# Performance work log

Hardware: AMD Instinct MI355X
Metric: run time of the kernel (lower is better)

Reference implementation:

```python
import jax, jax.numpy as jnp
import numpy as np

MP1, NX, P, HT, HE = 524288, 32768, 128, 128, 64


def setup_inputs() -> dict:
    key = jax.random.key(0)
    ks = jax.random.split(key, 12)
    w = lambda k, shape, fan_in: jax.random.normal(k, shape, jnp.float32) / np.sqrt(fan_in).astype(np.float32)
    a = jax.random.normal(ks[0], (MP1,), jnp.float32)
    x = jax.random.uniform(ks[1], (NX,), jnp.float32)
    t = jax.random.uniform(ks[2], (), jnp.float32)
    # DeepONet-style operator net: branch Linear(Mp1 -> p), trunk MLP (x,t) -> p
    Wb = w(ks[3], (P, MP1), MP1); bb = jnp.zeros((P,), jnp.float32)
    Wt1 = w(ks[4], (HT, 2), 2); bt1 = jnp.zeros((HT,), jnp.float32)
    Wt2 = w(ks[5], (HT, HT), HT); bt2 = jnp.zeros((HT,), jnp.float32)
    Wt3 = w(ks[6], (P, HT), HT); bt3 = jnp.zeros((P,), jnp.float32)
    # EnergyNet F(y,z): tiny smooth MLP R^2 -> R (needs 3rd-order derivatives)
    We1 = w(ks[7], (HE, 2), 2); be1 = jnp.zeros((HE,), jnp.float32)
    We2 = w(ks[8], (HE, HE), HE); be2 = jnp.zeros((HE,), jnp.float32)
    We3 = w(ks[9], (1, HE), HE); be3 = jnp.zeros((1,), jnp.float32)
    return dict(a=a, x=x, t=t, Wb=Wb, bb=bb, Wt1=Wt1, bt1=bt1, Wt2=Wt2, bt2=bt2,
                Wt3=Wt3, bt3=bt3, We1=We1, be1=be1, We2=We2, be2=be2, We3=We3, be3=be3)


def reference(a, x, t, Wb, bb, Wt1, bt1, Wt2, bt2, Wt3, bt3, We1, be1, We2, be2, We3, be3):
    # branch encoding of the input function a: (P,)
    b = Wb @ a + bb

    def u_fn(xi):  # scalar x -> scalar u(x, t)
        h = jnp.tanh(Wt1 @ jnp.stack([xi, t]) + bt1)
        h = jnp.tanh(Wt2 @ h + bt2)
        return jnp.dot(b, Wt3 @ h + bt3)

    def F(y, z):  # EnergyNet: scalar (y, z) -> scalar
        h = jnp.tanh(We1 @ jnp.stack([y, z]) + be1)
        h = jnp.tanh(We2 @ h + be2)
        return (We3 @ h + be3)[0]

    # u and its spatial derivatives, vmapped over the Nx grid points
    u = jax.vmap(u_fn)(x)
    u_x = jax.vmap(jax.grad(u_fn))(x)
    u_xx = jax.vmap(jax.grad(jax.grad(u_fn)))(x)
    u_xxx = jax.vmap(jax.grad(jax.grad(jax.grad(u_fn))))(x)

    # all needed partials of F(y, z), exactly as in the original module
    F_y = jax.grad(F)
    F_yz = jax.vmap(jax.grad(F_y, 1))(u, u_x)
    F_yy, F_yyz = jax.vmap(jax.value_and_grad(jax.grad(F_y), 1))(u, u_x)
    F_zz, (F_yzz, F_zzz) = jax.vmap(jax.value_and_grad(jax.grad(jax.grad(F, 1), 1), (0, 1)))(u, u_x)

    F_yx = F_yy * u_x + F_yz * u_xx
    F_zxx = (F_yz * u_xx + F_zz * u_xxx + F_yyz * u_x ** 2
             + 2.0 * F_yzz * u_x * u_xx + F_zzz * u_xx ** 2)
    return (-F_yx + F_zxx).reshape(x.shape[0])
```

## Files before the change

kernel.cpp:

```cpp
#include <hip/hip_runtime.h>
#include <cmath>

#define MP1 524288
#define NXP 32768

typedef float vfloat4 __attribute__((ext_vector_type(4)));


__global__ __launch_bounds__(256) void prep1_k(const float* __restrict__ Wt2,
                                               const float* __restrict__ We2,
                                               float* __restrict__ ws) {
    int idx = blockIdx.x * 256 + threadIdx.x;
    if (idx < 128) ws[idx] = 0.0f;
    if (idx < 16384) {
        int j = idx >> 7, k = idx & 127;
        ws[512 + k * 128 + j] = Wt2[idx];
    }
    if (idx < 4096) {
        int m = idx >> 6, i = idx & 63;
        ws[16896 + i * 64 + m] = We2[idx];
    }
}

__global__ __launch_bounds__(256) void gemv_k(const float* __restrict__ Wb,
                                              const float* __restrict__ a,
                                              float* __restrict__ b_acc) {
    const int row = blockIdx.x;
    const int chunk = blockIdx.y;
    const int t = threadIdx.x;
    size_t base = (size_t)row * MP1 + (size_t)chunk * 16384;
    const vfloat4* W4 = (const vfloat4*)(Wb + base);
    const float4* A4 = (const float4*)(a + (size_t)chunk * 16384);
    float sum = 0.0f;
#pragma unroll
    for (int it = 0; it < 16; ++it) {
        vfloat4 w = __builtin_nontemporal_load(&W4[t + it * 256]);
        float4 av = A4[t + it * 256];
        sum += w[0] * av.x + w[1] * av.y + w[2] * av.z + w[3] * av.w;
    }
#pragma unroll
    for (int off = 32; off > 0; off >>= 1) sum += __shfl_down(sum, off, 64);
    __shared__ float red[4];
    int wid = t >> 6;
    if ((t & 63) == 0) red[wid] = sum;
    __syncthreads();
    if (t == 0) atomicAdd(&b_acc[row], red[0] + red[1] + red[2] + red[3]);
}

__global__ __launch_bounds__(128) void prep2_k(const float* __restrict__ ws_in,
                                               const float* __restrict__ bb,
                                               const float* __restrict__ Wt3,
                                               const float* __restrict__ bt3,
                                               float* __restrict__ ws) {
    int k = threadIdx.x;
    float cv = 0.0f;
    for (int j = 0; j < 128; ++j)
        cv = fmaf(ws_in[j] + bb[j], Wt3[j * 128 + k], cv);
    ws[128 + k] = cv;
    float p = (ws_in[k] + bb[k]) * bt3[k];
#pragma unroll
    for (int off = 32; off > 0; off >>= 1) p += __shfl_down(p, off, 64);
    __shared__ float red[2];
    if ((k & 63) == 0) red[k >> 6] = p;
    __syncthreads();
    if (k == 0) ws[256] = red[0] + red[1];
}

#define SW_WT1 0
#define SW_BT1 256
#define SW_BT2 384
#define SW_CVEC 512
#define SW_WE1 640
#define SW_BE1 768
#define SW_BE2 832
#define SW_WE3 896
#define UREDP 960
#define H1V_ 1216
#define FREDP (H1V_ + 4096)
#define SCR_ 9408
#define LDSF 13504

__global__ __launch_bounds__(512, 4) void point_k(const float* __restrict__ x,
                                                  const float* __restrict__ tptr,
                                                  const float* __restrict__ Wt1,
                                                  const float* __restrict__ bt1,
                                                  const float* __restrict__ bt2,
                                                  const float* __restrict__ We1,
                                                  const float* __restrict__ be1,
                                                  const float* __restrict__ be2,
                                                  const float* __restrict__ We3,
                                                  const float* __restrict__ ws,
                                                  float* __restrict__ out) {
    __shared__ __align__(16) float lds[LDSF];
    const int tid = threadIdx.x;
    const int p = tid & 63;
    const int slice = __builtin_amdgcn_readfirstlane(tid >> 6);
    const int i = blockIdx.x * 64 + p;
    const float xi = x[i];
    const float tt = tptr[0];
    const float u_const = ws[256];

    if (tid < 256) lds[SW_WT1 + tid] = Wt1[tid];
    else if (tid < 384) lds[SW_BT1 + tid - 256] = bt1[tid - 256];
    else lds[SW_BT2 + tid - 384] = bt2[tid - 384];
    {
        int o = 512 + tid;
        if (o < 640) lds[o] = ws[128 + (o - 512)];
        else if (o < 768) lds[o] = We1[o - 640];
        else if (o < 832) lds[o] = be1[o - 768];
        else if (o < 896) lds[o] = be2[o - 832];
        else if (o < 960) lds[o] = We3[o - 896];
    }
    __syncthreads();

#pragma unroll
    for (int q = 0; q < 16; ++q) {
        int k = slice * 16 + q;
        float z = fmaf(lds[SW_WT1 + 2 * k], xi,
                       fmaf(lds[SW_WT1 + 2 * k + 1], tt, lds[SW_BT1 + k]));
        lds[H1V_ + k * 64 + p] = tanhf(z);
    }

    float a0[16], a1[16], a2[16], a3[16];
#pragma unroll
    for (int jj = 0; jj < 16; ++jj) { a0[jj] = 0.f; a1[jj] = 0.f; a2[jj] = 0.f; a3[jj] = 0.f; }
    for (int c = 0; c < 4; ++c) {
        __syncthreads();
        {
            const float4* src = (const float4*)(ws + 512 + c * 4096);
            float4* dst = (float4*)(lds + SCR_);
            dst[tid] = src[tid];
            dst[tid + 512] = src[tid + 512];
        }
        __syncthreads();
#pragma unroll 2
        for (int kl = 0; kl < 32; ++kl) {
            int k = c * 32 + kl;
            float v = lds[H1V_ + k * 64 + p];
            float w = lds[SW_WT1 + 2 * k];
            float s = 1.f - v * v;
            float f2 = -2.f * v * s;
            float f3 = 2.f * s * (2.f * v * v - s);
            float w2 = w * w;
            float d1 = s * w;
            float d2 = f2 * w2;
            float d3 = f3 * w2 * w;
            const float4* wr = (const float4*)(lds + SCR_ + kl * 128 + slice * 16);
            float4 wv0 = wr[0], wv1 = wr[1], wv2 = wr[2], wv3 = wr[3];
            const float wf[16] = {wv0.x, wv0.y, wv0.z, wv0.w, wv1.x, wv1.y, wv1.z, wv1.w,
                                  wv2.x, wv2.y, wv2.z, wv2.w, wv3.x, wv3.y, wv3.z, wv3.w};
#pragma unroll
            for (int jj = 0; jj < 16; ++jj) {
                float wjk = wf[jj];
                a0[jj] = fmaf(wjk, v, a0[jj]);
                a1[jj] = fmaf(wjk, d1, a1[jj]);
                a2[jj] = fmaf(wjk, d2, a2[jj]);
                a3[jj] = fmaf(wjk, d3, a3[jj]);
            }
        }
    }
    float u0 = 0.f, u1 = 0.f, u2 = 0.f, u3 = 0.f;
#pragma unroll
    for (int jj = 0; jj < 16; ++jj) {
        int j = slice * 16 + jj;
        float z0 = a0[jj] + lds[SW_BT2 + j];
        float z1 = a1[jj], z2 = a2[jj], z3 = a3[jj];
        float v = tanhf(z0);
        float s = 1.f - v * v;
        float f2 = -2.f * v * s;
        float f3 = 2.f * s * (2.f * v * v - s);
        float cj = lds[SW_CVEC + j];
        u0 = fmaf(cj, v, u0);
        u1 = fmaf(cj, s * z1, u1);
        u2 = fmaf(cj, f2 * z1 * z1 + s * z2, u2);
        u3 = fmaf(cj, f3 * z1 * z1 * z1 + 3.f * f2 * z1 * z2 + s * z3, u3);
    }
    __syncthreads();
    lds[SCR_ + 0 * 512 + slice * 64 + p] = u0;
    lds[SCR_ + 1 * 512 + slice * 64 + p] = u1;
    lds[SCR_ + 2 * 512 + slice * 64 + p] = u2;
    lds[SCR_ + 3 * 512 + slice * 64 + p] = u3;
    __syncthreads();

    if (tid < 64) {
        float r0 = u_const, r1 = 0.f, r2 = 0.f, r3 = 0.f;
#pragma unroll
        for (int s = 0; s < 8; ++s) {
            r0 += lds[SCR_ + 0 * 512 + s * 64 + tid];
            r1 += lds[SCR_ + 1 * 512 + s * 64 + tid];
            r2 += lds[SCR_ + 2 * 512 + s * 64 + tid];
            r3 += lds[SCR_ + 3 * 512 + s * 64 + tid];
        }
        lds[UREDP + 0 * 64 + tid] = r0;
        lds[UREDP + 1 * 64 + tid] = r1;
        lds[UREDP + 2 * 64 + tid] = r2;
        lds[UREDP + 3 * 64 + tid] = r3;
    }
    __syncthreads();

    {
        const float4* src = (const float4*)(ws + 16896);
        float4* dst = (float4*)(lds + SCR_);
        dst[tid] = src[tid];
        dst[tid + 512] = src[tid + 512];
    }
    const float y = lds[UREDP + 0 * 64 + p];
    const float z = lds[UREDP + 1 * 64 + p];
#pragma unroll
    for (int q = 0; q < 8; ++q) {
        int ii = slice * 8 + q;
        float g = fmaf(lds[SW_WE1 + 2 * ii], y,
                       fmaf(lds[SW_WE1 + 2 * ii + 1], z, lds[SW_BE1 + ii]));
        lds[H1V_ + ii * 64 + p] = tanhf(g);
    }
    __syncthreads();

    {
        float A0[8], A1[8], A2[8], A3[8], A4[8], A5[8], A6[8], A7[8], A8[8];
#pragma unroll
        for (int mm = 0; mm < 8; ++mm) {
            A0[mm] = 0.f; A1[mm] = 0.f; A2[mm] = 0.f; A3[mm] = 0.f; A4[mm] = 0.f;
            A5[mm] = 0.f; A6[mm] = 0.f; A7[mm] = 0.f; A8[mm] = 0.f;
        }
#pragma unroll 2
        for (int ii = 0; ii < 64; ++ii) {
            float v = lds[H1V_ + ii * 64 + p];
            float w0 = lds[SW_WE1 + 2 * ii];
            float w1 = lds[SW_WE1 + 2 * ii + 1];
            float s = 1.f - v * v;
            float f2 = -2.f * v * s;
            float f3 = 2.f * s * (2.f * v * v - s);
            float w00 = w0 * w0, w01 = w0 * w1, w11 = w1 * w1;
            float j1 = s * w0, j2 = s * w1;
            float j3 = f2 * w00, j4 = f2 * w01, j5 = f2 * w11;
            float j6 = f3 * w00 * w1, j7 = f3 * w01 * w1, j8 = f3 * w11 * w1;
            const float4* wr = (const float4*)(lds + SCR_ + ii * 64 + slice * 8);
            float4 wv0 = wr[0], wv1 = wr[1];
            const float wf[8] = {wv0.x, wv0.y, wv0.z, wv0.w, wv1.x, wv1.y, wv1.z, wv1.w};
#pragma unroll
            for (int mm = 0; mm < 8; ++mm) {
                float wmi = wf[mm];
                A0[mm] = fmaf(wmi, v,  A0[mm]);
                A1[mm] = fmaf(wmi, j1, A1[mm]);
                A2[mm] = fmaf(wmi, j2, A2[mm]);
                A3[mm] = fmaf(wmi, j3, A3[mm]);
                A4[mm] = fmaf(wmi, j4, A4[mm]);
                A5[mm] = fmaf(wmi, j5, A5[mm]);
                A6[mm] = fmaf(wmi, j6, A6[mm]);
                A7[mm] = fmaf(wmi, j7, A7[mm]);
                A8[mm] = fmaf(wmi, j8, A8[mm]);
            }
        }
        float Fyy = 0.f, Fyz = 0.f, Fzz = 0.f, Fyyz = 0.f, Fyzz = 0.f, Fzzz = 0.f;
#pragma unroll
        for (int mm = 0; mm < 8; ++mm) {
            int m = slice * 8 + mm;
            float G0 = A0[mm] + lds[SW_BE2 + m];
            float v = tanhf(G0);
            float s = 1.f - v * v;
            float f2 = -2.f * v * s;
            float f3 = 2.f * s * (2.f * v * v - s);
            float Gy = A1[mm], Gz = A2[mm];
            float Gyy = A3[mm], Gyz = A4[mm], Gzz = A5[mm];
            float Hyy = f2 * Gy * Gy + s * Gyy;
            float Hyz = f2 * Gy * Gz + s * Gyz;
            float Hzz = f2 * Gz * Gz + s * Gzz;
            float Hyyz = f3 * Gy * Gy * Gz + f2 * (Gyy * Gz + 2.f * Gyz * Gy) + s * A6[mm];
            float Hyzz = f3 * Gy * Gz * Gz + f2 * (2.f * Gyz * Gz + Gzz * Gy) + s * A7[mm];
            float Hzzz = f3 * Gz * Gz * Gz + 3.f * f2 * Gzz * Gz + s * A8[mm];
            float w3 = lds[SW_WE3 + m];
            Fyy  = fmaf(w3, Hyy,  Fyy);
            Fyz  = fmaf(w3, Hyz,  Fyz);
            Fzz  = fmaf(w3, Hzz,  Fzz);
            Fyyz = fmaf(w3, Hyyz, Fyyz);
            Fyzz = fmaf(w3, Hyzz, Fyzz);
            Fzzz = fmaf(w3, Hzzz, Fzzz);
        }
        lds[FREDP + 0 * 512 + slice * 64 + p] = Fyy;
        lds[FREDP + 1 * 512 + slice * 64 + p] = Fyz;
        lds[FREDP + 2 * 512 + slice * 64 + p] = Fzz;
        lds[FREDP + 3 * 512 + slice * 64 + p] = Fyyz;
        lds[FREDP + 4 * 512 + slice * 64 + p] = Fyzz;
        lds[FREDP + 5 * 512 + slice * 64 + p] = Fzzz;
    }
    __syncthreads();

    if (tid < 64) {
        float F[6] = {0.f, 0.f, 0.f, 0.f, 0.f, 0.f};
#pragma unroll
        for (int s = 0; s < 8; ++s) {
#pragma unroll
            for (int q = 0; q < 6; ++q) F[q] += lds[FREDP + q * 512 + s * 64 + tid];
        }
        float u1r = lds[UREDP + 1 * 64 + tid];
        float u2r = lds[UREDP + 2 * 64 + tid];
        float u3r = lds[UREDP + 3 * 64 + tid];
        float F_yx  = F[0] * u1r + F[1] * u2r;
        float F_zxx = F[1] * u2r + F[2] * u3r + F[3] * u1r * u1r
                    + 2.f * F[4] * u1r * u2r + F[5] * u2r * u2r;
        out[blockIdx.x * 64 + tid] = F_zxx - F_yx;
    }
}

extern "C" void kernel_launch(void* const* d_in, const int* in_sizes, int n_in,
                              void* d_out, int out_size, void* d_ws, size_t ws_size,
                              hipStream_t stream) {
    const float* a   = (const float*)d_in[0];
    const float* x   = (const float*)d_in[1];
    const float* t   = (const float*)d_in[2];
    const float* Wb  = (const float*)d_in[3];
    const float* bb  = (const float*)d_in[4];
    const float* Wt1 = (const float*)d_in[5];
    const float* bt1 = (const float*)d_in[6];
    const float* Wt2 = (const float*)d_in[7];
    const float* bt2 = (const float*)d_in[8];
    const float* Wt3 = (const float*)d_in[9];
    const float* bt3 = (const float*)d_in[10];
    const float* We1 = (const float*)d_in[11];
    const float* be1 = (const float*)d_in[12];
    const float* We2 = (const float*)d_in[13];
    const float* be2 = (const float*)d_in[14];
    const float* We3 = (const float*)d_in[15];

    float* ws = (float*)d_ws;
    float* out = (float*)d_out;

    prep1_k<<<64, 256, 0, stream>>>(Wt2, We2, ws);
    gemv_k<<<dim3(128, 32), 256, 0, stream>>>(Wb, a, ws);
    prep2_k<<<1, 128, 0, stream>>>(ws, bb, Wt3, bt3, ws);
    point_k<<<NXP / 64, 512, 0, stream>>>(x, t, Wt1, bt1, bt2, We1, be1, be2, We3,
                                          ws, out);
}
```

Before: 473.8 us.

## Merge prep kernels, drop atomics, use fast tanh and precompute EnergyNet weight products

Replaces the two prep kernels and the atomicAdd reduction with per-chunk partial sums that a single merged prep kernel reduces, removing one launch and the zero-init step. Swaps tanhf for an exp2/rcp-based fast tanh. Simplifies the derivative factors by pulling constants (-2, 2) out of the inner loops, and precomputes the We1 products into LDS. Also drops the inner-loop unroll factor to 1. The fast tanh approximation may shift accuracy slightly. The main cost is likely the 256MB Wb GEMV, so point-kernel savings may matter little.

```diff
diff --git a/kernel.cpp b/kernel.cpp
--- a/kernel.cpp
+++ b/kernel.cpp
@@ -6,25 +6,21 @@
 
 typedef float vfloat4 __attribute__((ext_vector_type(4)));
 
-
-__global__ __launch_bounds__(256) void prep1_k(const float* __restrict__ Wt2,
-                                               const float* __restrict__ We2,
-                                               float* __restrict__ ws) {
-    int idx = blockIdx.x * 256 + threadIdx.x;
-    if (idx < 128) ws[idx] = 0.0f;
-    if (idx < 16384) {
-        int j = idx >> 7, k = idx & 127;
-        ws[512 + k * 128 + j] = Wt2[idx];
-    }
-    if (idx < 4096) {
-        int m = idx >> 6, i = idx & 63;
-        ws[16896 + i * 64 + m] = We2[idx];
-    }
+#define PART_   0
+#define CVEC_   4096
+#define UCONST_ 4224
+#define WT2T_   8192
+#define WE2T_   24576
+
+__device__ __forceinline__ float tanh_fast(float x) {
+    x = fminf(20.f, fmaxf(-20.f, x));
+    float t = exp2f(x * 2.8853900817779268f);
+    return (t - 1.f) * __builtin_amdgcn_rcpf(t + 1.f);
 }
 
 __global__ __launch_bounds__(256) void gemv_k(const float* __restrict__ Wb,
                                               const float* __restrict__ a,
-                                              float* __restrict__ b_acc) {
+                                              float* __restrict__ ws) {
     const int row = blockIdx.x;
     const int chunk = blockIdx.y;
     const int t = threadIdx.x;
@@ -44,41 +40,62 @@
     int wid = t >> 6;
     if ((t & 63) == 0) red[wid] = sum;
     __syncthreads();
-    if (t == 0) atomicAdd(&b_acc[row], red[0] + red[1] + red[2] + red[3]);
-}
-
-__global__ __launch_bounds__(128) void prep2_k(const float* __restrict__ ws_in,
-                                               const float* __restrict__ bb,
-                                               const float* __restrict__ Wt3,
-                                               const float* __restrict__ bt3,
-                                               float* __restrict__ ws) {
-    int k = threadIdx.x;
-    float cv = 0.0f;
-    for (int j = 0; j < 128; ++j)
-        cv = fmaf(ws_in[j] + bb[j], Wt3[j * 128 + k], cv);
-    ws[128 + k] = cv;
-    float p = (ws_in[k] + bb[k]) * bt3[k];
-#pragma unroll
-    for (int off = 32; off > 0; off >>= 1) p += __shfl_down(p, off, 64);
-    __shared__ float red[2];
-    if ((k & 63) == 0) red[k >> 6] = p;
-    __syncthreads();
-    if (k == 0) ws[256] = red[0] + red[1];
+    if (t == 0) ws[PART_ + row * 32 + chunk] = red[0] + red[1] + red[2] + red[3];
+}
+
+__global__ __launch_bounds__(256) void prep_k(const float* __restrict__ bb,
+                                              const float* __restrict__ Wt2,
+                                              const float* __restrict__ We2,
+                                              const float* __restrict__ Wt3,
+                                              const float* __restrict__ bt3,
+                                              float* __restrict__ ws) {
+    const int tid = threadIdx.x;
+    if (blockIdx.x == 0) {
+        __shared__ float sh[128];
+        __shared__ float red[2];
+        if (tid < 128) {
+            float b = bb[tid];
+            const float* part = ws + PART_ + tid * 32;
+#pragma unroll
+            for (int c = 0; c < 32; ++c) b += part[c];
+            sh[tid] = b;
+        }
+        __syncthreads();
+        if (tid < 128) {
+            float cv = 0.f;
+            for (int j = 0; j < 128; ++j) cv = fmaf(sh[j], Wt3[j * 128 + tid], cv);
+            ws[CVEC_ + tid] = cv;
+            float p = sh[tid] * bt3[tid];
+#pragma unroll
+            for (int off = 32; off > 0; off >>= 1) p += __shfl_down(p, off, 64);
+            if ((tid & 63) == 0) red[tid >> 6] = p;
+        }
+        __syncthreads();
+        if (tid == 0) ws[UCONST_] = red[0] + red[1];
+    } else {
+        int idx = (blockIdx.x - 1) * 256 + tid;
+        int j = idx >> 7, k = idx & 127;
+        ws[WT2T_ + k * 128 + j] = Wt2[idx];
+        if (idx < 4096) {
+            int m = idx >> 6, i2 = idx & 63;
+            ws[WE2T_ + i2 * 64 + m] = We2[idx];
+        }
+    }
 }
 
 #define SW_WT1 0
 #define SW_BT1 256
 #define SW_BT2 384
 #define SW_CVEC 512
-#define SW_WE1 640
-#define SW_BE1 768
-#define SW_BE2 832
-#define SW_WE3 896
-#define UREDP 960
-#define H1V_ 1216
+#define SW_WE1X 640
+#define SW_BE1 1152
+#define SW_BE2 1216
+#define SW_WE3 1280
+#define UREDP 1344
+#define H1V_ 1600
 #define FREDP (H1V_ + 4096)
-#define SCR_ 9408
-#define LDSF 13504
+#define SCR_ 9792
+#define LDSF 13888
 
 __global__ __launch_bounds__(512, 4) void point_k(const float* __restrict__ x,
                                                   const float* __restrict__ tptr,
@@ -98,18 +115,22 @@
     const int i = blockIdx.x * 64 + p;
     const float xi = x[i];
     const float tt = tptr[0];
-    const float u_const = ws[256];
+    const float u_const = ws[UCONST_];
 
     if (tid < 256) lds[SW_WT1 + tid] = Wt1[tid];
     else if (tid < 384) lds[SW_BT1 + tid - 256] = bt1[tid - 256];
     else lds[SW_BT2 + tid - 384] = bt2[tid - 384];
-    {
-        int o = 512 + tid;
-        if (o < 640) lds[o] = ws[128 + (o - 512)];
-        else if (o < 768) lds[o] = We1[o - 640];
-        else if (o < 832) lds[o] = be1[o - 768];
-        else if (o < 896) lds[o] = be2[o - 832];
-        else if (o < 960) lds[o] = We3[o - 896];
+    if (tid < 128) lds[SW_CVEC + tid] = ws[CVEC_ + tid];
+    else if (tid < 192) lds[SW_BE1 + tid - 128] = be1[tid - 128];
+    else if (tid < 256) lds[SW_BE2 + tid - 192] = be2[tid - 192];
+    else if (tid < 320) lds[SW_WE3 + tid - 256] = We3[tid - 256];
+    else if (tid < 384) {
+        int ii = tid - 320;
+        float w0 = We1[2 * ii], w1 = We1[2 * ii + 1];
+        float w00 = w0 * w0, w01 = w0 * w1, w11 = w1 * w1;
+        float* X = lds + SW_WE1X + ii * 8;
+        X[0] = w0; X[1] = w1; X[2] = w00; X[3] = w01; X[4] = w11;
+        X[5] = w00 * w1; X[6] = w01 * w1; X[7] = w11 * w1;
     }
     __syncthreads();
 
@@ -118,7 +139,7 @@
         int k = slice * 16 + q;
         float z = fmaf(lds[SW_WT1 + 2 * k], xi,
                        fmaf(lds[SW_WT1 + 2 * k + 1], tt, lds[SW_BT1 + k]));
-        lds[H1V_ + k * 64 + p] = tanhf(z);
+        lds[H1V_ + k * 64 + p] = tanh_fast(z);
     }
 
     float a0[16], a1[16], a2[16], a3[16];
@@ -127,24 +148,25 @@
     for (int c = 0; c < 4; ++c) {
         __syncthreads();
         {
-            const float4* src = (const float4*)(ws + 512 + c * 4096);
+            const float4* src = (const float4*)(ws + WT2T_ + c * 4096);
             float4* dst = (float4*)(lds + SCR_);
             dst[tid] = src[tid];
             dst[tid + 512] = src[tid + 512];
         }
         __syncthreads();
-#pragma unroll 2
+#pragma unroll 1
         for (int kl = 0; kl < 32; ++kl) {
             int k = c * 32 + kl;
             float v = lds[H1V_ + k * 64 + p];
             float w = lds[SW_WT1 + 2 * k];
-            float s = 1.f - v * v;
-            float f2 = -2.f * v * s;
-            float f3 = 2.f * s * (2.f * v * v - s);
-            float w2 = w * w;
+            float s = fmaf(-v, v, 1.f);
+            float t2 = v * s;
+            float m = fmaf(-3.f, s, 2.f);
+            float sm = s * m;
+            float w2 = w * w, w3 = w2 * w;
             float d1 = s * w;
-            float d2 = f2 * w2;
-            float d3 = f3 * w2 * w;
+            float d2 = t2 * w2;
+            float d3 = sm * w3;
             const float4* wr = (const float4*)(lds + SCR_ + kl * 128 + slice * 16);
             float4 wv0 = wr[0], wv1 = wr[1], wv2 = wr[2], wv3 = wr[3];
             const float wf[16] = {wv0.x, wv0.y, wv0.z, wv0.w, wv1.x, wv1.y, wv1.z, wv1.w,
@@ -164,8 +186,8 @@
     for (int jj = 0; jj < 16; ++jj) {
         int j = slice * 16 + jj;
         float z0 = a0[jj] + lds[SW_BT2 + j];
-        float z1 = a1[jj], z2 = a2[jj], z3 = a3[jj];
-        float v = tanhf(z0);
+        float z1 = a1[jj], z2 = -2.f * a2[jj], z3 = 2.f * a3[jj];
+        float v = tanh_fast(z0);
         float s = 1.f - v * v;
         float f2 = -2.f * v * s;
         float f3 = 2.f * s * (2.f * v * v - s);
@@ -199,7 +221,7 @@
     __syncthreads();
 
     {
-        const float4* src = (const float4*)(ws + 16896);
+        const float4* src = (const float4*)(ws + WE2T_);
         float4* dst = (float4*)(lds + SCR_);
         dst[tid] = src[tid];
         dst[tid + 512] = src[tid + 512];
@@ -209,9 +231,9 @@
 #pragma unroll
     for (int q = 0; q < 8; ++q) {
         int ii = slice * 8 + q;
-        float g = fmaf(lds[SW_WE1 + 2 * ii], y,
-                       fmaf(lds[SW_WE1 + 2 * ii + 1], z, lds[SW_BE1 + ii]));
-        lds[H1V_ + ii * 64 + p] = tanhf(g);
+        float g = fmaf(lds[SW_WE1X + ii * 8], y,
+                       fmaf(lds[SW_WE1X + ii * 8 + 1], z, lds[SW_BE1 + ii]));
+        lds[H1V_ + ii * 64 + p] = tanh_fast(g);
     }
     __syncthreads();
 
@@ -222,18 +244,18 @@
             A0[mm] = 0.f; A1[mm] = 0.f; A2[mm] = 0.f; A3[mm] = 0.f; A4[mm] = 0.f;
             A5[mm] = 0.f; A6[mm] = 0.f; A7[mm] = 0.f; A8[mm] = 0.f;
         }
-#pragma unroll 2
+#pragma unroll 1
         for (int ii = 0; ii < 64; ++ii) {
             float v = lds[H1V_ + ii * 64 + p];
-            float w0 = lds[SW_WE1 + 2 * ii];
-            float w1 = lds[SW_WE1 + 2 * ii + 1];
-            float s = 1.f - v * v;
-            float f2 = -2.f * v * s;
-            float f3 = 2.f * s * (2.f * v * v - s);
-            float w00 = w0 * w0, w01 = w0 * w1, w11 = w1 * w1;
-            float j1 = s * w0, j2 = s * w1;
-            float j3 = f2 * w00, j4 = f2 * w01, j5 = f2 * w11;
-            float j6 = f3 * w00 * w1, j7 = f3 * w01 * w1, j8 = f3 * w11 * w1;
+            const float4* xw = (const float4*)(lds + SW_WE1X + ii * 8);
+            float4 xa = xw[0], xb = xw[1];
+            float s = fmaf(-v, v, 1.f);
+            float t2 = v * s;
+            float m = fmaf(-3.f, s, 2.f);
+            float sm = s * m;
+            float j1 = s * xa.x, j2 = s * xa.y;
+            float j3 = t2 * xa.z, j4 = t2 * xa.w, j5 = t2 * xb.x;
+            float j6 = sm * xb.y, j7 = sm * xb.z, j8 = sm * xb.w;
             const float4* wr = (const float4*)(lds + SCR_ + ii * 64 + slice * 8);
             float4 wv0 = wr[0], wv1 = wr[1];
             const float wf[8] = {wv0.x, wv0.y, wv0.z, wv0.w, wv1.x, wv1.y, wv1.z, wv1.w};
@@ -256,18 +278,19 @@
         for (int mm = 0; mm < 8; ++mm) {
             int m = slice * 8 + mm;
             float G0 = A0[mm] + lds[SW_BE2 + m];
-            float v = tanhf(G0);
+            float v = tanh_fast(G0);
             float s = 1.f - v * v;
             float f2 = -2.f * v * s;
             float f3 = 2.f * s * (2.f * v * v - s);
             float Gy = A1[mm], Gz = A2[mm];
-            float Gyy = A3[mm], Gyz = A4[mm], Gzz = A5[mm];
+            float Gyy = -2.f * A3[mm], Gyz = -2.f * A4[mm], Gzz = -2.f * A5[mm];
+            float Gyyz = 2.f * A6[mm], Gyzz = 2.f * A7[mm], Gzzz = 2.f * A8[mm];
             float Hyy = f2 * Gy * Gy + s * Gyy;
             float Hyz = f2 * Gy * Gz + s * Gyz;
             float Hzz = f2 * Gz * Gz + s * Gzz;
-            float Hyyz = f3 * Gy * Gy * Gz + f2 * (Gyy * Gz + 2.f * Gyz * Gy) + s * A6[mm];
-            float Hyzz = f3 * Gy * Gz * Gz + f2 * (2.f * Gyz * Gz + Gzz * Gy) + s * A7[mm];
-            float Hzzz = f3 * Gz * Gz * Gz + 3.f * f2 * Gzz * Gz + s * A8[mm];
+            float Hyyz = f3 * Gy * Gy * Gz + f2 * (Gyy * Gz + 2.f * Gyz * Gy) + s * Gyyz;
+            float Hyzz = f3 * Gy * Gz * Gz + f2 * (2.f * Gyz * Gz + Gzz * Gy) + s * Gyzz;
+            float Hzzz = f3 * Gz * Gz * Gz + 3.f * f2 * Gzz * Gz + s * Gzzz;
             float w3 = lds[SW_WE3 + m];
             Fyy  = fmaf(w3, Hyy,  Fyy);
             Fyz  = fmaf(w3, Hyz,  Fyz);
@@ -325,9 +348,8 @@
     float* ws = (float*)d_ws;
     float* out = (float*)d_out;
 
-    prep1_k<<<64, 256, 0, stream>>>(Wt2, We2, ws);
     gemv_k<<<dim3(128, 32), 256, 0, stream>>>(Wb, a, ws);
-    prep2_k<<<1, 128, 0, stream>>>(ws, bb, Wt3, bt3, ws);
+    prep_k<<<65, 256, 0, stream>>>(bb, Wt2, We2, Wt3, bt3, ws);
     point_k<<<NXP / 64, 512, 0, stream>>>(x, t, Wt1, bt1, bt2, We1, be1, be2, We3,
                                           ws, out);
 }
```

New measurement: 460.8 us. 1.03x faster.
